# Optimization experiments

Hardware: AMD Instinct MI355X
Metric: run time of the kernel (lower is better)

The kernel has to match this reference:

```python
import jax, jax.numpy as jnp
import numpy as np

B, S, D_IN, D_OUT = 4, 2048, 2048, 2048
EPS = 1e-10


def setup_inputs() -> dict:
    key = jax.random.key(0)
    kx, kw, kb = jax.random.split(key, 3)
    x = jax.random.normal(kx, (B, S, D_IN), dtype=jnp.float32)
    weight = jax.random.normal(kw, (D_OUT, D_IN), dtype=jnp.float32) * 0.02
    bias = jax.random.normal(kb, (D_OUT,), dtype=jnp.float32) * 0.02
    return {"x": x, "weight": weight, "bias": bias}


def reference(x, weight, bias):
    # abs-mean scale over the whole weight matrix (scalar)
    scale = jnp.mean(jnp.abs(weight))
    # ternary quantization: round(w/scale) clamped to {-1, 0, 1}
    w_t = jnp.clip(jnp.round(weight / (scale + EPS)), -1.0, 1.0)
    # straight-through estimator: forward uses w_t*scale, grad flows to weight
    w_ste = weight + jax.lax.stop_gradient(w_t * scale - weight)
    # F.linear: x @ w_ste.T + bias
    return jnp.einsum('bsi,oi->bso', x, w_ste) + bias
```

## Files before the change

### kernel.cpp

```cpp
#include <hip/hip_runtime.h>
#include <hip/hip_bf16.h>
#include <stdint.h>

#define M_DIM 8192
#define N_DIM 2048
#define K_DIM 2048
#define NT    (K_DIM / 64)

typedef float f32x4 __attribute__((ext_vector_type(4)));
typedef short bf16x8 __attribute__((ext_vector_type(8)));

typedef const __attribute__((address_space(1))) char* gp_t;
typedef __attribute__((address_space(3))) char* lp_t;

static __device__ __forceinline__ void gload_lds16(const void* g, void* l) {
  __builtin_amdgcn_global_load_lds((gp_t)(uintptr_t)g, (lp_t)(uint32_t)(uintptr_t)l, 16, 0, 0);
}

static __device__ __forceinline__ unsigned short f2bf(float f) {
  unsigned int u = __float_as_uint(f);
  unsigned int r = (u + 0x7FFFu + ((u >> 16) & 1u)) >> 16;
  return (unsigned short)r;
}

__global__ void cvt_x_absum(const float* __restrict__ x, unsigned short* __restrict__ xb,
                            const float* __restrict__ w, float* __restrict__ partials) {
  const int b = blockIdx.x;
  if (b < 16384) {
    int tid = b * 256 + threadIdx.x;
    float4 v = ((const float4*)x)[tid];
    ushort4 o;
    o.x = f2bf(v.x); o.y = f2bf(v.y); o.z = f2bf(v.z); o.w = f2bf(v.w);
    ((ushort4*)xb)[tid] = o;
  } else {
    int tid = (b - 16384) * 256 + threadIdx.x;
    const float4* w4 = (const float4*)w;
    float s = 0.f;
#pragma unroll
    for (int i = 0; i < 4; ++i) {
      float4 v = w4[tid + i * 262144];
      s += fabsf(v.x) + fabsf(v.y) + fabsf(v.z) + fabsf(v.w);
    }
#pragma unroll
    for (int off = 32; off > 0; off >>= 1) s += __shfl_down(s, off, 64);
    __shared__ float ls[4];
    if ((threadIdx.x & 63) == 0) ls[threadIdx.x >> 6] = s;
    __syncthreads();
    if (threadIdx.x == 0) partials[b - 16384] = (ls[0] + ls[1]) + (ls[2] + ls[3]);
  }
}

__global__ void quant_w(const float* __restrict__ w, const float* __restrict__ partials,
                        unsigned short* __restrict__ wt, float* __restrict__ scale_out) {
  __shared__ float ls[4];
  float s = 0.f;
#pragma unroll
  for (int i = 0; i < 4; ++i) s += partials[threadIdx.x + i * 256];
#pragma unroll
  for (int off = 32; off > 0; off >>= 1) s += __shfl_down(s, off, 64);
  if ((threadIdx.x & 63) == 0) ls[threadIdx.x >> 6] = s;
  __syncthreads();
  const float scale = ((ls[0] + ls[1]) + (ls[2] + ls[3])) * (1.0f / 4194304.0f);
  if (blockIdx.x == 0 && threadIdx.x == 0) scale_out[0] = scale;

  const float inv = 1.0f / (scale + 1e-10f);
  int tid = blockIdx.x * 256 + threadIdx.x;
  float4 v = ((const float4*)w)[tid];
  ushort4 o;
  float t;
  t = fminf(1.f, fmaxf(-1.f, rintf(v.x * inv))); o.x = f2bf(t);
  t = fminf(1.f, fmaxf(-1.f, rintf(v.y * inv))); o.y = f2bf(t);
  t = fminf(1.f, fmaxf(-1.f, rintf(v.z * inv))); o.z = f2bf(t);
  t = fminf(1.f, fmaxf(-1.f, rintf(v.w * inv))); o.w = f2bf(t);
  ((ushort4*)wt)[tid] = o;
}


#define VMCNT(n) asm volatile("s_waitcnt vmcnt(" #n ")" ::: "memory")
#define FENCE    asm volatile("" ::: "memory")
#define BARRIER  do { FENCE; __builtin_amdgcn_s_barrier(); FENCE; } while (0)

#define READ_A(mh)                                                                              \
  do {                                                                                          \
    _Pragma("unroll") for (int i = 0; i < 4; ++i) {                                             \
      a_r[i][0] = *(const bf16x8*)(curA + (wr * 128 + (mh) * 64 + i * 16) * 128 + rd0);         \
      a_r[i][1] = *(const bf16x8*)(curA + (wr * 128 + (mh) * 64 + i * 16) * 128 + rd1);         \
    }                                                                                           \
  } while (0)

#define READ_B(nh, br)                                                                          \
  do {                                                                                          \
    _Pragma("unroll") for (int j = 0; j < 2; ++j) {                                             \
      br[j][0] = *(const bf16x8*)(curB + (wc * 64 + (nh) * 32 + j * 16) * 128 + rd0);           \
      br[j][1] = *(const bf16x8*)(curB + (wc * 64 + (nh) * 32 + j * 16) * 128 + rd1);           \
    }                                                                                           \
  } while (0)

#define MFMA_PH(mh, nh, br)                                                                     \
  do {                                                                                          \
    __builtin_amdgcn_s_setprio(1);                                                              \
    _Pragma("unroll") for (int i = 0; i < 4; ++i)                                               \
      _Pragma("unroll") for (int j = 0; j < 2; ++j)                                             \
        acc[(mh) * 4 + i][(nh) * 2 + j] = __builtin_amdgcn_mfma_f32_16x16x32_bf16(              \
            a_r[i][0], br[j][0], acc[(mh) * 4 + i][(nh) * 2 + j], 0, 0, 0);                     \
    _Pragma("unroll") for (int i = 0; i < 4; ++i)                                               \
      _Pragma("unroll") for (int j = 0; j < 2; ++j)                                             \
        acc[(mh) * 4 + i][(nh) * 2 + j] = __builtin_amdgcn_mfma_f32_16x16x32_bf16(              \
            a_r[i][1], br[j][1], acc[(mh) * 4 + i][(nh) * 2 + j], 0, 0, 0);                     \
    __builtin_amdgcn_s_setprio(0);                                                              \
  } while (0)

#define SA(bufsel, r) gload_lds16(Ag + offA[r] + ktA, ldsb + (bufsel) * 65536 + tid * 16 + (r) * 8192)
#define SB(bufsel, r) gload_lds16(Bg + offB[r] + ktB, ldsb + (bufsel) * 65536 + 32768 + tid * 16 + (r) * 8192)

__global__ void __launch_bounds__(512, 2)
gemm_bt(const unsigned short* __restrict__ A, const unsigned short* __restrict__ Bt,
        const float* __restrict__ bias, const float* __restrict__ scale_p,
        float* __restrict__ out) {
  __shared__ __align__(16) char lds_raw[131072];
  char* ldsb = (char*)lds_raw;

  const int tid = threadIdx.x;
  const int lane = tid & 63;
  const int wid = tid >> 6;
  const int wr = wid >> 2;
  const int wc = wid & 3;
  const int l15 = lane & 15, lhi = lane >> 4;

  const int swzl = (l15 & 7) << 4;
  const int rd0 = l15 * 128 + ((lhi * 16) ^ swzl);
  const int rd1 = l15 * 128 + (((lhi * 16) ^ 64) ^ swzl);

  const int bid = blockIdx.x;
  const int swz = (bid & 7) * 32 + (bid >> 3);
  const int bm = swz >> 3;
  const int bn = swz & 7;
  const int m0 = bm << 8, n0 = bn << 8;

  const int srow = tid >> 3;
  const int scol = (((tid & 7) ^ ((tid >> 3) & 7)) << 4);
  const char* Ag = (const char*)A;
  const char* Bg = (const char*)Bt;
  uint32_t offA[4], offB[4];
#pragma unroll
  for (int r = 0; r < 4; ++r) {
    offA[r] = (uint32_t)(m0 + srow + r * 64) * (K_DIM * 2) + scol;
    offB[r] = (uint32_t)(n0 + srow + r * 64) * (K_DIM * 2) + scol;
  }
  uint32_t ktA = 0, ktB = 0;

  f32x4 acc[8][4];
#pragma unroll
  for (int m = 0; m < 8; ++m)
#pragma unroll
    for (int n = 0; n < 4; ++n) {
      f32x4 z = {0.f, 0.f, 0.f, 0.f};
      acc[m][n] = z;
    }

  SA(0, 0); SA(0, 1); SA(0, 2); SA(0, 3);
  SB(0, 0); SB(0, 1); SB(0, 2); SB(0, 3);
  ktB = 128;
  SB(1, 0); SB(1, 1); SB(1, 2); SB(1, 3);
  ktA = 128; ktB = 256;
  VMCNT(4);
  BARRIER;

  bf16x8 a_r[4][2], b0[2][2], b1[2][2];

  for (int t = 0; t < NT; ++t) {
    const int cb = t & 1;
    const char* curA = ldsb + cb * 65536;
    const char* curB = curA + 32768;

    READ_A(0);
    READ_B(0, b0);
    if (t < NT - 1) { SA(cb ^ 1, 0); SA(cb ^ 1, 1); }
    MFMA_PH(0, 0, b0);

    READ_B(1, b1);
    if (t < NT - 1) { SA(cb ^ 1, 2); SA(cb ^ 1, 3); ktA += 128; }
    MFMA_PH(0, 1, b1);

    BARRIER;

    READ_A(1);
    if (t < NT - 2) { SB(cb, 0); SB(cb, 1); }
    MFMA_PH(1, 0, b0);

    if (t < NT - 2) {
      SB(cb, 2); SB(cb, 3); ktB += 128;
      VMCNT(4);
    } else {
      VMCNT(0);
    }
    MFMA_PH(1, 1, b1);

    BARRIER;
  }

  const float scale = scale_p[0];
#pragma unroll
  for (int n = 0; n < 4; ++n) {
    const int col = n0 + wc * 64 + n * 16 + l15;
    const float bv = bias[col];
#pragma unroll
    for (int m = 0; m < 8; ++m) {
      const int r0 = m0 + wr * 128 + m * 16 + lhi * 4;
      float* op = out + (size_t)r0 * N_DIM + col;
#pragma unroll
      for (int j = 0; j < 4; ++j) op[(size_t)j * N_DIM] = acc[m][n][j] * scale + bv;
    }
  }
}

extern "C" void kernel_launch(void* const* d_in, const int* in_sizes, int n_in,
                              void* d_out, int out_size, void* d_ws, size_t ws_size,
                              hipStream_t stream) {
  (void)in_sizes; (void)n_in; (void)out_size; (void)ws_size;
  const float* x    = (const float*)d_in[0];
  const float* w    = (const float*)d_in[1];
  const float* bias = (const float*)d_in[2];
  float* out = (float*)d_out;

  float* partials = (float*)d_ws;
  float* scale_slot = partials + 1024;
  unsigned short* wt = (unsigned short*)((char*)d_ws + 8192);
  unsigned short* xb = (unsigned short*)((char*)d_ws + 8192 + (size_t)N_DIM * K_DIM * 2);

  cvt_x_absum<<<17408, 256, 0, stream>>>(x, xb, w, partials);
  quant_w<<<4096, 256, 0, stream>>>(w, partials, wt, scale_slot);
  gemm_bt<<<256, 512, 0, stream>>>(xb, wt, bias, scale_slot, out);
}
```

Before: 83.92 us.

## Double-buffer LDS fragment registers and prefetch next tile's first A/B fragments

Adds separate register sets for the two A halves and reorders the main loop so the next K-tile's first A and B fragments are read from LDS during the current tile's second-half MFMAs. The aim is to hide LDS read latency behind matrix math instead of stalling at the start of each iteration. To make the next buffer safe to read, a full vmcnt(0) wait now sits before the mid-loop barrier. That wait can expose the global-to-LDS load latency that the earlier partial wait left in flight. The extra fragment registers also raise VGPR pressure under the 512-thread, 2-blocks-per-CU launch bound.

```diff
diff --git a/kernel.cpp b/kernel.cpp
--- a/kernel.cpp
+++ b/kernel.cpp
@@ -80,33 +80,33 @@
 #define FENCE    asm volatile("" ::: "memory")
 #define BARRIER  do { FENCE; __builtin_amdgcn_s_barrier(); FENCE; } while (0)
 
-#define READ_A(mh)                                                                              \
+#define READ_A_TO(base, mh, dst)                                                                \
   do {                                                                                          \
     _Pragma("unroll") for (int i = 0; i < 4; ++i) {                                             \
-      a_r[i][0] = *(const bf16x8*)(curA + (wr * 128 + (mh) * 64 + i * 16) * 128 + rd0);         \
-      a_r[i][1] = *(const bf16x8*)(curA + (wr * 128 + (mh) * 64 + i * 16) * 128 + rd1);         \
+      dst[i][0] = *(const bf16x8*)((base) + (wr * 128 + (mh) * 64 + i * 16) * 128 + rd0);       \
+      dst[i][1] = *(const bf16x8*)((base) + (wr * 128 + (mh) * 64 + i * 16) * 128 + rd1);       \
     }                                                                                           \
   } while (0)
 
-#define READ_B(nh, br)                                                                          \
+#define READ_B_TO(base, nh, dst)                                                                \
   do {                                                                                          \
     _Pragma("unroll") for (int j = 0; j < 2; ++j) {                                             \
-      br[j][0] = *(const bf16x8*)(curB + (wc * 64 + (nh) * 32 + j * 16) * 128 + rd0);           \
-      br[j][1] = *(const bf16x8*)(curB + (wc * 64 + (nh) * 32 + j * 16) * 128 + rd1);           \
+      dst[j][0] = *(const bf16x8*)((base) + (wc * 64 + (nh) * 32 + j * 16) * 128 + rd0);        \
+      dst[j][1] = *(const bf16x8*)((base) + (wc * 64 + (nh) * 32 + j * 16) * 128 + rd1);        \
     }                                                                                           \
   } while (0)
 
-#define MFMA_PH(mh, nh, br)                                                                     \
+#define MFMA_Q(mh, nh, ar, br)                                                                  \
   do {                                                                                          \
     __builtin_amdgcn_s_setprio(1);                                                              \
     _Pragma("unroll") for (int i = 0; i < 4; ++i)                                               \
       _Pragma("unroll") for (int j = 0; j < 2; ++j)                                             \
         acc[(mh) * 4 + i][(nh) * 2 + j] = __builtin_amdgcn_mfma_f32_16x16x32_bf16(              \
-            a_r[i][0], br[j][0], acc[(mh) * 4 + i][(nh) * 2 + j], 0, 0, 0);                     \
+            ar[i][0], br[j][0], acc[(mh) * 4 + i][(nh) * 2 + j], 0, 0, 0);                      \
     _Pragma("unroll") for (int i = 0; i < 4; ++i)                                               \
       _Pragma("unroll") for (int j = 0; j < 2; ++j)                                             \
         acc[(mh) * 4 + i][(nh) * 2 + j] = __builtin_amdgcn_mfma_f32_16x16x32_bf16(              \
-            a_r[i][1], br[j][1], acc[(mh) * 4 + i][(nh) * 2 + j], 0, 0, 0);                     \
+            ar[i][1], br[j][1], acc[(mh) * 4 + i][(nh) * 2 + j], 0, 0, 0);                      \
     __builtin_amdgcn_s_setprio(0);                                                              \
   } while (0)
 
@@ -166,35 +166,40 @@
   VMCNT(4);
   BARRIER;
 
-  bf16x8 a_r[4][2], b0[2][2], b1[2][2];
+  bf16x8 a0[4][2], a1[4][2], b0[2][2], b1[2][2];
+
+  {
+    const char* c0A = ldsb;
+    const char* c0B = ldsb + 32768;
+    READ_A_TO(c0A, 0, a0);
+    READ_B_TO(c0B, 0, b0);
+  }
 
   for (int t = 0; t < NT; ++t) {
     const int cb = t & 1;
     const char* curA = ldsb + cb * 65536;
     const char* curB = curA + 32768;
-
-    READ_A(0);
-    READ_B(0, b0);
+    const char* nxtA = ldsb + (cb ^ 1) * 65536;
+    const char* nxtB = nxtA + 32768;
+
+    READ_B_TO(curB, 1, b1);
     if (t < NT - 1) { SA(cb ^ 1, 0); SA(cb ^ 1, 1); }
-    MFMA_PH(0, 0, b0);
-
-    READ_B(1, b1);
+    MFMA_Q(0, 0, a0, b0);
+
+    READ_A_TO(curA, 1, a1);
     if (t < NT - 1) { SA(cb ^ 1, 2); SA(cb ^ 1, 3); ktA += 128; }
-    MFMA_PH(0, 1, b1);
-
+    MFMA_Q(0, 1, a0, b1);
+
+    VMCNT(0);
     BARRIER;
 
-    READ_A(1);
+    if (t < NT - 1) READ_A_TO(nxtA, 0, a0);
     if (t < NT - 2) { SB(cb, 0); SB(cb, 1); }
-    MFMA_PH(1, 0, b0);
-
-    if (t < NT - 2) {
-      SB(cb, 2); SB(cb, 3); ktB += 128;
-      VMCNT(4);
-    } else {
-      VMCNT(0);
-    }
-    MFMA_PH(1, 1, b1);
+    MFMA_Q(1, 0, a1, b0);
+    if (t < NT - 1) READ_B_TO(nxtB, 0, b0);
+
+    if (t < NT - 2) { SB(cb, 2); SB(cb, 3); ktB += 128; }
+    MFMA_Q(1, 1, a1, b1);
 
     BARRIER;
   }
```

After: 87.60 us. 1.04x slower.
